# Kernel optimization log

Measured on AMD Instinct MI355X. Metric: run time of the kernel, lower is better.

Reference implementation:

```python
import jax, jax.numpy as jnp
import numpy as np

N_NODES = 50000


def gcn_conv(x, src, dst, W, b):
    # PyG GCNConv: x @ W, symmetric gcn_norm with self-loops, scatter-add, + bias
    n = x.shape[0]
    x = x @ W  # [N, out]
    deg = jax.ops.segment_sum(jnp.ones_like(src, dtype=x.dtype), dst, num_segments=n)
    dinv = jnp.where(deg > 0, deg ** -0.5, 0.0)
    norm = dinv[src] * dinv[dst]  # [E+N]
    out = jax.ops.segment_sum(x[src] * norm[:, None], dst, num_segments=n)
    return out + b


def setup_inputs() -> dict:
    key = jax.random.key(0)
    ks = jax.random.split(key, 8)
    x = jax.random.normal(ks[0], (N_NODES, 128), dtype=jnp.float32)
    edge_index = jax.random.randint(ks[1], (2, 800000), 0, N_NODES, dtype=jnp.int64)
    def glorot(k, fan_in, fan_out):
        s = (6.0 / (fan_in + fan_out)) ** 0.5
        return jax.random.uniform(k, (fan_in, fan_out), jnp.float32, -s, s)
    return {
        "x": x,
        "edge_index": edge_index,
        "W1": glorot(ks[2], 128, 128), "b1": jnp.zeros((128,), jnp.float32),
        "W2": glorot(ks[3], 128, 128), "b2": jnp.zeros((128,), jnp.float32),
        "W3": glorot(ks[4], 128, 64), "b3": jnp.zeros((64,), jnp.float32),
    }


def reference(x, edge_index, W1, b1, W2, b2, W3, b3):
    n = x.shape[0]
    loops = jnp.arange(n, dtype=edge_index.dtype)
    src = jnp.concatenate([edge_index[0], loops])  # self-loops appended
    dst = jnp.concatenate([edge_index[1], loops])
    h = gcn_conv(x, src, dst, W1, b1)
    h = jax.nn.relu(h)  # dropout is identity in eval mode
    h = gcn_conv(h, src, dst, W2, b2)
    h = jax.nn.relu(h)
    h = gcn_conv(h, src, dst, W3, b3)
    return h
```

## Files before the change

### kernel.cpp

```cpp
#include <hip/hip_runtime.h>
#include <hip/hip_bf16.h>
#include <hip/hip_fp16.h>


typedef __attribute__((ext_vector_type(8))) short s16x8;
typedef __attribute__((ext_vector_type(8))) unsigned short u16x8;
typedef __attribute__((ext_vector_type(4))) float f32x4;

__device__ __forceinline__ float bfu_lo(uint v) { return __uint_as_float(v << 16); }
__device__ __forceinline__ float bfu_hi(uint v) { return __uint_as_float(v & 0xffff0000u); }
__device__ __forceinline__ float dec_norm(uint m) {
    return __half2float(__ushort_as_half((ushort)(m >> 16)));
}
__device__ __forceinline__ ushort bf16_bits(float f) {
    union { __hip_bfloat16 h; ushort u; } x;
    x.h = __float2bfloat16(f);
    return x.u;
}


__global__ void k_init(int* __restrict__ deg, int n,
                       uint4* __restrict__ ep4, int cap4) {
    int i = blockIdx.x * blockDim.x + threadIdx.x;
    if (i < n) deg[i] = 1;
    if (i < cap4) ep4[i] = make_uint4(0u, 0u, 0u, 0u);
}

__global__ void k_hist(const int* __restrict__ dst, int E,
                       int* __restrict__ deg, ushort* __restrict__ rank) {
    int e = blockIdx.x * blockDim.x + threadIdx.x;
    if (e < E) {
        int r = atomicAdd(&deg[dst[e]], 1);
        rank[e] = (ushort)r;
    }
}

__global__ void k_scan_block(const int* __restrict__ deg, int* __restrict__ offs,
                             int* __restrict__ bsum, float* __restrict__ dinv, int n) {
    __shared__ int sm[256];
    int tid = threadIdx.x;
    int i = blockIdx.x * 256 + tid;
    int v = (i < n) ? deg[i] : 0;
    int pv = (i < n) ? ((v + 7) & ~7) : 0;
    if (i < n) dinv[i] = rsqrtf((float)v);
    sm[tid] = pv;
    __syncthreads();
    for (int off = 1; off < 256; off <<= 1) {
        int t = (tid >= off) ? sm[tid - off] : 0;
        __syncthreads();
        sm[tid] += t;
        __syncthreads();
    }
    if (i < n) offs[i] = sm[tid] - pv;
    if (tid == 255) bsum[blockIdx.x] = sm[255];
}

__global__ void k_scan_bsum(int* __restrict__ bsum, int nb, int* __restrict__ offs, int n) {
    __shared__ int sm[256];
    int tid = threadIdx.x;
    int v = (tid < nb) ? bsum[tid] : 0;
    sm[tid] = v;
    __syncthreads();
    for (int off = 1; off < 256; off <<= 1) {
        int t = (tid >= off) ? sm[tid - off] : 0;
        __syncthreads();
        sm[tid] += t;
        __syncthreads();
    }
    if (tid < nb) bsum[tid] = sm[tid] - v;
    if (tid == 255) offs[n] = sm[255];
}

__global__ void k_add_bsum(int* __restrict__ offs, const int* __restrict__ bsum, int n) {
    int i = blockIdx.x * blockDim.x + threadIdx.x;
    if (i < n) offs[i] += bsum[i >> 8];
}

__global__ __launch_bounds__(256) void k_fill(const int* __restrict__ src,
                                              const int* __restrict__ dst,
                                              const ushort* __restrict__ rank,
                                              int E, int n,
                                              const int* __restrict__ offs,
                                              const float* __restrict__ dinv,
                                              uint* __restrict__ ep) {
    int e = blockIdx.x * blockDim.x + threadIdx.x;
    int tot = E + n;
    if (e >= tot) return;
    int s, d, r;
    if (e < E) {
        s = src[e];
        d = dst[e];
        r = rank[e];
    } else {
        s = d = e - E;
        r = 0;
    }
    int pos = offs[d] + r;
    uint hb = (uint)__half_as_ushort(__float2half(dinv[s] * dinv[d]));
    ep[pos] = (hb << 16) | (uint)s;
}

__global__ void k_transW(const float* __restrict__ W1, const float* __restrict__ W2,
                         const float* __restrict__ W3,
                         ushort* __restrict__ Wt1, ushort* __restrict__ Wt2,
                         ushort* __restrict__ Wt3) {
    int i = blockIdx.x * 256 + threadIdx.x;
    if (i < 128 * 128) {
        int r = i >> 7, c = i & 127;
        Wt1[c * 128 + r] = bf16_bits(W1[i]);
        Wt2[c * 128 + r] = bf16_bits(W2[i]);
    }
    if (i < 128 * 64) {
        int r = i >> 6, c = i & 63;
        Wt3[c * 128 + r] = bf16_bits(W3[i]);
    }
}

template <int OUT, bool ABF16>
__global__ __launch_bounds__(256) void k_gemm_mfma(const void* __restrict__ Ain,
                                                   const ushort* __restrict__ Wt,
                                                   ushort* __restrict__ To, int n) {
    constexpr int NT = OUT / 16;
    __shared__ ushort As[64][136];
    __shared__ ushort Ws[OUT][136];
    const int tid = threadIdx.x;
    const int wave = tid >> 6, lane = tid & 63;
    const int m0 = blockIdx.x * 64;

#pragma unroll
    for (int it = 0; it < OUT / 16; ++it) {
        int idx = it * 256 + tid;
        int r = idx >> 4;
        int c8 = (idx & 15) << 3;
        *(u16x8*)&Ws[r][c8] = *(const u16x8*)(Wt + r * 128 + c8);
    }
    if constexpr (ABF16) {
        const ushort* A = (const ushort*)Ain;
#pragma unroll
        for (int it = 0; it < 4; ++it) {
            int idx = it * 256 + tid;
            int r = idx >> 4;
            int c8 = (idx & 15) << 3;
            u16x8 v = {0, 0, 0, 0, 0, 0, 0, 0};
            if (m0 + r < n) v = *(const u16x8*)(A + (size_t)(m0 + r) * 128 + c8);
            *(u16x8*)&As[r][c8] = v;
        }
    } else {
        const float* A = (const float*)Ain;
#pragma unroll
        for (int it = 0; it < 8; ++it) {
            int idx = it * 256 + tid;
            int r = idx >> 5;
            int c4 = (idx & 31) << 2;
            float4 v = make_float4(0.f, 0.f, 0.f, 0.f);
            if (m0 + r < n) v = *(const float4*)(A + (size_t)(m0 + r) * 128 + c4);
            As[r][c4 + 0] = bf16_bits(v.x);
            As[r][c4 + 1] = bf16_bits(v.y);
            As[r][c4 + 2] = bf16_bits(v.z);
            As[r][c4 + 3] = bf16_bits(v.w);
        }
    }
    __syncthreads();

    const int lrow = lane & 15;
    const int kgrp = lane >> 4;

    s16x8 a[4];
#pragma unroll
    for (int kk = 0; kk < 4; ++kk)
        a[kk] = *(const s16x8*)&As[wave * 16 + lrow][kk * 32 + kgrp * 8];

    f32x4 acc[NT];
#pragma unroll
    for (int nt = 0; nt < NT; ++nt) {
        f32x4 c = {0.f, 0.f, 0.f, 0.f};
#pragma unroll
        for (int kk = 0; kk < 4; ++kk) {
            s16x8 b = *(const s16x8*)&Ws[nt * 16 + lrow][kk * 32 + kgrp * 8];
            c = __builtin_amdgcn_mfma_f32_16x16x32_bf16(a[kk], b, c, 0, 0, 0);
        }
        acc[nt] = c;
    }

#pragma unroll
    for (int j = 0; j < 4; ++j) {
        int row = m0 + wave * 16 + kgrp * 4 + j;
        if (row < n) {
#pragma unroll
            for (int nt = 0; nt < NT; ++nt)
                To[(size_t)row * OUT + nt * 16 + lrow] = bf16_bits(acc[nt][j]);
        }
    }
}

template <bool RELU>
__global__ __launch_bounds__(256) void k_agg128(const ushort* __restrict__ T,
                                                const int* __restrict__ offs,
                                                const uint* __restrict__ ep,
                                                const float* __restrict__ bias,
                                                uint* __restrict__ outq, int n) {
    int pr = blockIdx.x * 4 + (threadIdx.x >> 6);
    int lane = threadIdx.x & 63;
    int w0 = pr * 2;
    if (w0 >= n) return;
    int w1 = w0 + 1;
    bool has1 = (w1 < n);
    int eA = offs[w0], endA = offs[w0 + 1];
    int eB = has1 ? offs[w1] : 0;
    int endB = has1 ? offs[w1 + 1] : 0;

    const uint* Tl = (const uint*)T + lane;
    const uint4 z4 = make_uint4(0u, 0u, 0u, 0u);
    float a0 = 0.f, a1 = 0.f, c0 = 0.f, c1 = 0.f;

    uint4 mA0 = *(const uint4*)(ep + eA);
    uint4 mA1 = *(const uint4*)(ep + eA + 4);
    uint4 mB0 = z4, mB1 = z4;
    if (eB < endB) { mB0 = *(const uint4*)(ep + eB); mB1 = *(const uint4*)(ep + eB + 4); }

    for (;;) {
        uint rA0 = Tl[(size_t)(mA0.x & 0xffffu) * 64];
        uint rA1 = Tl[(size_t)(mA0.y & 0xffffu) * 64];
        uint rA2 = Tl[(size_t)(mA0.z & 0xffffu) * 64];
        uint rA3 = Tl[(size_t)(mA0.w & 0xffffu) * 64];
        uint rA4 = Tl[(size_t)(mA1.x & 0xffffu) * 64];
        uint rA5 = Tl[(size_t)(mA1.y & 0xffffu) * 64];
        uint rA6 = Tl[(size_t)(mA1.z & 0xffffu) * 64];
        uint rA7 = Tl[(size_t)(mA1.w & 0xffffu) * 64];
        uint rB0 = Tl[(size_t)(mB0.x & 0xffffu) * 64];
        uint rB1 = Tl[(size_t)(mB0.y & 0xffffu) * 64];
        uint rB2 = Tl[(size_t)(mB0.z & 0xffffu) * 64];
        uint rB3 = Tl[(size_t)(mB0.w & 0xffffu) * 64];
        uint rB4 = Tl[(size_t)(mB1.x & 0xffffu) * 64];
        uint rB5 = Tl[(size_t)(mB1.y & 0xffffu) * 64];
        uint rB6 = Tl[(size_t)(mB1.z & 0xffffu) * 64];
        uint rB7 = Tl[(size_t)(mB1.w & 0xffffu) * 64];
        float wA0 = dec_norm(mA0.x), wA1 = dec_norm(mA0.y);
        float wA2 = dec_norm(mA0.z), wA3 = dec_norm(mA0.w);
        float wA4 = dec_norm(mA1.x), wA5 = dec_norm(mA1.y);
        float wA6 = dec_norm(mA1.z), wA7 = dec_norm(mA1.w);
        float wB0 = dec_norm(mB0.x), wB1 = dec_norm(mB0.y);
        float wB2 = dec_norm(mB0.z), wB3 = dec_norm(mB0.w);
        float wB4 = dec_norm(mB1.x), wB5 = dec_norm(mB1.y);
        float wB6 = dec_norm(mB1.z), wB7 = dec_norm(mB1.w);
        eA += 8;
        eB += 8;
        bool moreA = (eA < endA), moreB = (eB < endB);
        if (moreA) { mA0 = *(const uint4*)(ep + eA); mA1 = *(const uint4*)(ep + eA + 4); }
        else       { mA0 = z4; mA1 = z4; }
        if (moreB) { mB0 = *(const uint4*)(ep + eB); mB1 = *(const uint4*)(ep + eB + 4); }
        else       { mB0 = z4; mB1 = z4; }
        a0 += wA0 * bfu_lo(rA0); a1 += wA0 * bfu_hi(rA0);
        a0 += wA1 * bfu_lo(rA1); a1 += wA1 * bfu_hi(rA1);
        a0 += wA2 * bfu_lo(rA2); a1 += wA2 * bfu_hi(rA2);
        a0 += wA3 * bfu_lo(rA3); a1 += wA3 * bfu_hi(rA3);
        a0 += wA4 * bfu_lo(rA4); a1 += wA4 * bfu_hi(rA4);
        a0 += wA5 * bfu_lo(rA5); a1 += wA5 * bfu_hi(rA5);
        a0 += wA6 * bfu_lo(rA6); a1 += wA6 * bfu_hi(rA6);
        a0 += wA7 * bfu_lo(rA7); a1 += wA7 * bfu_hi(rA7);
        c0 += wB0 * bfu_lo(rB0); c1 += wB0 * bfu_hi(rB0);
        c0 += wB1 * bfu_lo(rB1); c1 += wB1 * bfu_hi(rB1);
        c0 += wB2 * bfu_lo(rB2); c1 += wB2 * bfu_hi(rB2);
        c0 += wB3 * bfu_lo(rB3); c1 += wB3 * bfu_hi(rB3);
        c0 += wB4 * bfu_lo(rB4); c1 += wB4 * bfu_hi(rB4);
        c0 += wB5 * bfu_lo(rB5); c1 += wB5 * bfu_hi(rB5);
        c0 += wB6 * bfu_lo(rB6); c1 += wB6 * bfu_hi(rB6);
        c0 += wB7 * bfu_lo(rB7); c1 += wB7 * bfu_hi(rB7);
        if (!moreA && !moreB) break;
    }

    float2 b = *(const float2*)(bias + (lane << 1));
    a0 += b.x; a1 += b.y;
    if (RELU) { a0 = fmaxf(a0, 0.f); a1 = fmaxf(a1, 0.f); }
    outq[(size_t)w0 * 64 + lane] = ((uint)bf16_bits(a1) << 16) | (uint)bf16_bits(a0);
    if (has1) {
        c0 += b.x; c1 += b.y;
        if (RELU) { c0 = fmaxf(c0, 0.f); c1 = fmaxf(c1, 0.f); }
        outq[(size_t)w1 * 64 + lane] = ((uint)bf16_bits(c1) << 16) | (uint)bf16_bits(c0);
    }
}

__global__ __launch_bounds__(256) void k_agg64(const ushort* __restrict__ T,
                                               const int* __restrict__ offs,
                                               const uint* __restrict__ ep,
                                               const float* __restrict__ bias,
                                               float* __restrict__ out, int n) {
    int pr = blockIdx.x * 4 + (threadIdx.x >> 6);
    int lane = threadIdx.x & 63;
    int w0 = pr * 2;
    if (w0 >= n) return;
    int w1 = w0 + 1;
    bool has1 = (w1 < n);
    int eA = offs[w0], endA = offs[w0 + 1];
    int eB = has1 ? offs[w1] : 0;
    int endB = has1 ? offs[w1 + 1] : 0;

    const ushort* Tl = T + lane;
    const uint4 z4 = make_uint4(0u, 0u, 0u, 0u);
    float a0 = 0.f, c0 = 0.f;

    uint4 mA0 = *(const uint4*)(ep + eA);
    uint4 mA1 = *(const uint4*)(ep + eA + 4);
    uint4 mB0 = z4, mB1 = z4;
    if (eB < endB) { mB0 = *(const uint4*)(ep + eB); mB1 = *(const uint4*)(ep + eB + 4); }

    for (;;) {
        float rA0 = __uint_as_float((uint)Tl[(size_t)(mA0.x & 0xffffu) * 64] << 16);
        float rA1 = __uint_as_float((uint)Tl[(size_t)(mA0.y & 0xffffu) * 64] << 16);
        float rA2 = __uint_as_float((uint)Tl[(size_t)(mA0.z & 0xffffu) * 64] << 16);
        float rA3 = __uint_as_float((uint)Tl[(size_t)(mA0.w & 0xffffu) * 64] << 16);
        float rA4 = __uint_as_float((uint)Tl[(size_t)(mA1.x & 0xffffu) * 64] << 16);
        float rA5 = __uint_as_float((uint)Tl[(size_t)(mA1.y & 0xffffu) * 64] << 16);
        float rA6 = __uint_as_float((uint)Tl[(size_t)(mA1.z & 0xffffu) * 64] << 16);
        float rA7 = __uint_as_float((uint)Tl[(size_t)(mA1.w & 0xffffu) * 64] << 16);
        float rB0 = __uint_as_float((uint)Tl[(size_t)(mB0.x & 0xffffu) * 64] << 16);
        float rB1 = __uint_as_float((uint)Tl[(size_t)(mB0.y & 0xffffu) * 64] << 16);
        float rB2 = __uint_as_float((uint)Tl[(size_t)(mB0.z & 0xffffu) * 64] << 16);
        float rB3 = __uint_as_float((uint)Tl[(size_t)(mB0.w & 0xffffu) * 64] << 16);
        float rB4 = __uint_as_float((uint)Tl[(size_t)(mB1.x & 0xffffu) * 64] << 16);
        float rB5 = __uint_as_float((uint)Tl[(size_t)(mB1.y & 0xffffu) * 64] << 16);
        float rB6 = __uint_as_float((uint)Tl[(size_t)(mB1.z & 0xffffu) * 64] << 16);
        float rB7 = __uint_as_float((uint)Tl[(size_t)(mB1.w & 0xffffu) * 64] << 16);
        float wA0 = dec_norm(mA0.x), wA1 = dec_norm(mA0.y);
        float wA2 = dec_norm(mA0.z), wA3 = dec_norm(mA0.w);
        float wA4 = dec_norm(mA1.x), wA5 = dec_norm(mA1.y);
        float wA6 = dec_norm(mA1.z), wA7 = dec_norm(mA1.w);
        float wB0 = dec_norm(mB0.x), wB1 = dec_norm(mB0.y);
        float wB2 = dec_norm(mB0.z), wB3 = dec_norm(mB0.w);
        float wB4 = dec_norm(mB1.x), wB5 = dec_norm(mB1.y);
        float wB6 = dec_norm(mB1.z), wB7 = dec_norm(mB1.w);
        eA += 8;
        eB += 8;
        bool moreA = (eA < endA), moreB = (eB < endB);
        if (moreA) { mA0 = *(const uint4*)(ep + eA); mA1 = *(const uint4*)(ep + eA + 4); }
        else       { mA0 = z4; mA1 = z4; }
        if (moreB) { mB0 = *(const uint4*)(ep + eB); mB1 = *(const uint4*)(ep + eB + 4); }
        else       { mB0 = z4; mB1 = z4; }
        a0 += wA0 * rA0 + wA1 * rA1 + wA2 * rA2 + wA3 * rA3;
        a0 += wA4 * rA4 + wA5 * rA5 + wA6 * rA6 + wA7 * rA7;
        c0 += wB0 * rB0 + wB1 * rB1 + wB2 * rB2 + wB3 * rB3;
        c0 += wB4 * rB4 + wB5 * rB5 + wB6 * rB6 + wB7 * rB7;
        if (!moreA && !moreB) break;
    }

    float bv = bias[lane];
    out[(size_t)w0 * 64 + lane] = a0 + bv;
    if (has1) out[(size_t)w1 * 64 + lane] = c0 + bv;
}


extern "C" void kernel_launch(void* const* d_in, const int* in_sizes, int n_in,
                              void* d_out, int out_size, void* d_ws, size_t ws_size,
                              hipStream_t stream) {
    const int n = in_sizes[0] / 128;
    const int E = in_sizes[1] / 2;

    const float* x  = (const float*)d_in[0];
    const int*   ei = (const int*)d_in[1];
    const float* W1 = (const float*)d_in[2];
    const float* b1 = (const float*)d_in[3];
    const float* W2 = (const float*)d_in[4];
    const float* b2 = (const float*)d_in[5];
    const float* W3 = (const float*)d_in[6];
    const float* b3 = (const float*)d_in[7];
    const int* src = ei;
    const int* dst = ei + E;
    float* out = (float*)d_out;

    const int cap = E + 8 * n;

    char* w = (char*)d_ws;
    auto alloc = [&](size_t bytes) {
        char* p = w;
        w += (bytes + 255) & ~(size_t)255;
        return p;
    };
    int*    deg    = (int*)alloc((size_t)n * 4);
    int*    offs   = (int*)alloc((size_t)(n + 1) * 4);
    int*    bsum   = (int*)alloc(256 * 4);
    float*  dinv   = (float*)alloc((size_t)n * 4);
    ushort* rank   = (ushort*)alloc((size_t)E * 2);
    uint*   ep     = (uint*)alloc((size_t)cap * 4);
    ushort* tA     = (ushort*)alloc((size_t)n * 128 * 2);
    uint*   hB     = (uint*)alloc((size_t)n * 64 * 4);
    ushort* Wt1    = (ushort*)alloc(128 * 128 * 2);
    ushort* Wt2    = (ushort*)alloc(128 * 128 * 2);
    ushort* Wt3    = (ushort*)alloc(64 * 128 * 2);

    const int nb = (n + 255) / 256;

    const int cap4 = (cap + 3) / 4;
    k_init<<<(cap4 + 255) / 256, 256, 0, stream>>>(deg, n, (uint4*)ep, cap4);
    k_transW<<<64, 256, 0, stream>>>(W1, W2, W3, Wt1, Wt2, Wt3);
    k_hist<<<(E + 255) / 256, 256, 0, stream>>>(dst, E, deg, rank);
    k_scan_block<<<nb, 256, 0, stream>>>(deg, offs, bsum, dinv, n);
    k_scan_bsum<<<1, 256, 0, stream>>>(bsum, nb, offs, n);
    k_add_bsum<<<nb, 256, 0, stream>>>(offs, bsum, n);
    k_fill<<<(E + n + 255) / 256, 256, 0, stream>>>(src, dst, rank, E, n, offs, dinv, ep);

    const int pair_blocks = ((n + 1) / 2 + 3) / 4;
    const int gemm_blocks = (n + 63) / 64;

    k_gemm_mfma<128, false><<<gemm_blocks, 256, 0, stream>>>(x, Wt1, tA, n);
    k_agg128<true><<<pair_blocks, 256, 0, stream>>>(tA, offs, ep, b1, hB, n);

    k_gemm_mfma<128, true><<<gemm_blocks, 256, 0, stream>>>(hB, Wt2, tA, n);
    k_agg128<true><<<pair_blocks, 256, 0, stream>>>(tA, offs, ep, b2, hB, n);

    k_gemm_mfma<64, true><<<gemm_blocks, 256, 0, stream>>>(hB, Wt3, tA, n);
    k_agg64<<<pair_blocks, 256, 0, stream>>>(tA, offs, ep, b3, out, n);
}
```

Measured before the change: 187.6 us.

## Fuse weight transpose into init, self-loops into scan, vectorize hist/fill and agg64

Merges the weight-transpose kernel into the init kernel. Self-loop CSR entries are now written in the offset-add pass, so the fill kernel handles only real edges, two per thread. The histogram also processes two edges per thread with vector loads. The final 64-wide aggregation now has each half-wave handle two destination nodes, loading two bf16 features per 32-bit gather. This cuts launch count and halves gather instructions in the last layer, at the cost of more register pressure and a less regular thread layout.

```diff
diff --git a/kernel.cpp b/kernel.cpp
--- a/kernel.cpp
+++ b/kernel.cpp
@@ -18,20 +18,37 @@
     return x.u;
 }
 
-
-__global__ void k_init(int* __restrict__ deg, int n,
+__global__ void k_init(const float* __restrict__ W1, const float* __restrict__ W2,
+                       const float* __restrict__ W3,
+                       ushort* __restrict__ Wt1, ushort* __restrict__ Wt2,
+                       ushort* __restrict__ Wt3,
+                       int* __restrict__ deg, int n,
                        uint4* __restrict__ ep4, int cap4) {
     int i = blockIdx.x * blockDim.x + threadIdx.x;
     if (i < n) deg[i] = 1;
     if (i < cap4) ep4[i] = make_uint4(0u, 0u, 0u, 0u);
+    if (i < 128 * 128) {
+        int r = i >> 7, c = i & 127;
+        Wt1[c * 128 + r] = bf16_bits(W1[i]);
+        Wt2[c * 128 + r] = bf16_bits(W2[i]);
+    }
+    if (i < 128 * 64) {
+        int r = i >> 6, c = i & 63;
+        Wt3[c * 128 + r] = bf16_bits(W3[i]);
+    }
 }
 
 __global__ void k_hist(const int* __restrict__ dst, int E,
                        int* __restrict__ deg, ushort* __restrict__ rank) {
-    int e = blockIdx.x * blockDim.x + threadIdx.x;
-    if (e < E) {
-        int r = atomicAdd(&deg[dst[e]], 1);
-        rank[e] = (ushort)r;
+    int e2 = (blockIdx.x * blockDim.x + threadIdx.x) * 2;
+    if (e2 >= E) return;
+    int2 d2 = *(const int2*)(dst + e2);
+    int r0 = atomicAdd(&deg[d2.x], 1);
+    if (e2 + 1 < E) {
+        int r1 = atomicAdd(&deg[d2.y], 1);
+        *(ushort2*)(rank + e2) = make_ushort2((ushort)r0, (ushort)r1);
+    } else {
+        rank[e2] = (ushort)r0;
     }
 }
 
@@ -71,48 +88,39 @@
     if (tid == 255) offs[n] = sm[255];
 }
 
-__global__ void k_add_bsum(int* __restrict__ offs, const int* __restrict__ bsum, int n) {
+__global__ void k_add_bsum(int* __restrict__ offs, const int* __restrict__ bsum,
+                           const float* __restrict__ dinv, uint* __restrict__ ep, int n) {
     int i = blockIdx.x * blockDim.x + threadIdx.x;
-    if (i < n) offs[i] += bsum[i >> 8];
+    if (i < n) {
+        int o = offs[i] + bsum[i >> 8];
+        offs[i] = o;
+        float dv = dinv[i];
+        uint hb = (uint)__half_as_ushort(__float2half(dv * dv));
+        ep[o] = (hb << 16) | (uint)i;
+    }
 }
 
 __global__ __launch_bounds__(256) void k_fill(const int* __restrict__ src,
                                               const int* __restrict__ dst,
                                               const ushort* __restrict__ rank,
-                                              int E, int n,
+                                              int E,
                                               const int* __restrict__ offs,
                                               const float* __restrict__ dinv,
                                               uint* __restrict__ ep) {
-    int e = blockIdx.x * blockDim.x + threadIdx.x;
-    int tot = E + n;
-    if (e >= tot) return;
-    int s, d, r;
-    if (e < E) {
-        s = src[e];
-        d = dst[e];
-        r = rank[e];
-    } else {
-        s = d = e - E;
-        r = 0;
-    }
-    int pos = offs[d] + r;
-    uint hb = (uint)__half_as_ushort(__float2half(dinv[s] * dinv[d]));
-    ep[pos] = (hb << 16) | (uint)s;
-}
-
-__global__ void k_transW(const float* __restrict__ W1, const float* __restrict__ W2,
-                         const float* __restrict__ W3,
-                         ushort* __restrict__ Wt1, ushort* __restrict__ Wt2,
-                         ushort* __restrict__ Wt3) {
-    int i = blockIdx.x * 256 + threadIdx.x;
-    if (i < 128 * 128) {
-        int r = i >> 7, c = i & 127;
-        Wt1[c * 128 + r] = bf16_bits(W1[i]);
-        Wt2[c * 128 + r] = bf16_bits(W2[i]);
-    }
-    if (i < 128 * 64) {
-        int r = i >> 6, c = i & 63;
-        Wt3[c * 128 + r] = bf16_bits(W3[i]);
+    int e2 = (blockIdx.x * blockDim.x + threadIdx.x) * 2;
+    if (e2 >= E) return;
+    int2 s2 = *(const int2*)(src + e2);
+    int2 d2 = *(const int2*)(dst + e2);
+    ushort2 r2 = *(const ushort2*)(rank + e2);
+    {
+        int pos = offs[d2.x] + (int)r2.x;
+        uint hb = (uint)__half_as_ushort(__float2half(dinv[s2.x] * dinv[d2.x]));
+        ep[pos] = (hb << 16) | (uint)s2.x;
+    }
+    if (e2 + 1 < E) {
+        int pos = offs[d2.y] + (int)r2.y;
+        uint hb = (uint)__half_as_ushort(__float2half(dinv[s2.y] * dinv[d2.y]));
+        ep[pos] = (hb << 16) | (uint)s2.y;
     }
 }
 
@@ -285,42 +293,43 @@
                                                const uint* __restrict__ ep,
                                                const float* __restrict__ bias,
                                                float* __restrict__ out, int n) {
-    int pr = blockIdx.x * 4 + (threadIdx.x >> 6);
+    int wv = blockIdx.x * 4 + (threadIdx.x >> 6);
     int lane = threadIdx.x & 63;
-    int w0 = pr * 2;
-    if (w0 >= n) return;
-    int w1 = w0 + 1;
-    bool has1 = (w1 < n);
-    int eA = offs[w0], endA = offs[w0 + 1];
-    int eB = has1 ? offs[w1] : 0;
-    int endB = has1 ? offs[w1 + 1] : 0;
-
-    const ushort* Tl = T + lane;
+    int half = lane >> 5;
+    int lh = lane & 31;
+    int base = wv * 4;
+    if (base >= n) return;
+    int wA = base + half * 2;
+    int wB = wA + 1;
+    int eA = 0, endA = 0, eB = 0, endB = 0;
+    if (wA < n) { eA = offs[wA]; endA = offs[wA + 1]; }
+    if (wB < n) { eB = offs[wB]; endB = offs[wB + 1]; }
+
+    const uint* Tl = (const uint*)T + lh;
     const uint4 z4 = make_uint4(0u, 0u, 0u, 0u);
-    float a0 = 0.f, c0 = 0.f;
-
-    uint4 mA0 = *(const uint4*)(ep + eA);
-    uint4 mA1 = *(const uint4*)(ep + eA + 4);
-    uint4 mB0 = z4, mB1 = z4;
+    float a0 = 0.f, a1 = 0.f, c0 = 0.f, c1 = 0.f;
+
+    uint4 mA0 = z4, mA1 = z4, mB0 = z4, mB1 = z4;
+    if (eA < endA) { mA0 = *(const uint4*)(ep + eA); mA1 = *(const uint4*)(ep + eA + 4); }
     if (eB < endB) { mB0 = *(const uint4*)(ep + eB); mB1 = *(const uint4*)(ep + eB + 4); }
 
     for (;;) {
-        float rA0 = __uint_as_float((uint)Tl[(size_t)(mA0.x & 0xffffu) * 64] << 16);
-        float rA1 = __uint_as_float((uint)Tl[(size_t)(mA0.y & 0xffffu) * 64] << 16);
-        float rA2 = __uint_as_float((uint)Tl[(size_t)(mA0.z & 0xffffu) * 64] << 16);
-        float rA3 = __uint_as_float((uint)Tl[(size_t)(mA0.w & 0xffffu) * 64] << 16);
-        float rA4 = __uint_as_float((uint)Tl[(size_t)(mA1.x & 0xffffu) * 64] << 16);
-        float rA5 = __uint_as_float((uint)Tl[(size_t)(mA1.y & 0xffffu) * 64] << 16);
-        float rA6 = __uint_as_float((uint)Tl[(size_t)(mA1.z & 0xffffu) * 64] << 16);
-        float rA7 = __uint_as_float((uint)Tl[(size_t)(mA1.w & 0xffffu) * 64] << 16);
-        float rB0 = __uint_as_float((uint)Tl[(size_t)(mB0.x & 0xffffu) * 64] << 16);
-        float rB1 = __uint_as_float((uint)Tl[(size_t)(mB0.y & 0xffffu) * 64] << 16);
-        float rB2 = __uint_as_float((uint)Tl[(size_t)(mB0.z & 0xffffu) * 64] << 16);
-        float rB3 = __uint_as_float((uint)Tl[(size_t)(mB0.w & 0xffffu) * 64] << 16);
-        float rB4 = __uint_as_float((uint)Tl[(size_t)(mB1.x & 0xffffu) * 64] << 16);
-        float rB5 = __uint_as_float((uint)Tl[(size_t)(mB1.y & 0xffffu) * 64] << 16);
-        float rB6 = __uint_as_float((uint)Tl[(size_t)(mB1.z & 0xffffu) * 64] << 16);
-        float rB7 = __uint_as_float((uint)Tl[(size_t)(mB1.w & 0xffffu) * 64] << 16);
+        uint rA0 = Tl[(size_t)(mA0.x & 0xffffu) * 32];
+        uint rA1 = Tl[(size_t)(mA0.y & 0xffffu) * 32];
+        uint rA2 = Tl[(size_t)(mA0.z & 0xffffu) * 32];
+        uint rA3 = Tl[(size_t)(mA0.w & 0xffffu) * 32];
+        uint rA4 = Tl[(size_t)(mA1.x & 0xffffu) * 32];
+        uint rA5 = Tl[(size_t)(mA1.y & 0xffffu) * 32];
+        uint rA6 = Tl[(size_t)(mA1.z & 0xffffu) * 32];
+        uint rA7 = Tl[(size_t)(mA1.w & 0xffffu) * 32];
+        uint rB0 = Tl[(size_t)(mB0.x & 0xffffu) * 32];
+        uint rB1 = Tl[(size_t)(mB0.y & 0xffffu) * 32];
+        uint rB2 = Tl[(size_t)(mB0.z & 0xffffu) * 32];
+        uint rB3 = Tl[(size_t)(mB0.w & 0xffffu) * 32];
+        uint rB4 = Tl[(size_t)(mB1.x & 0xffffu) * 32];
+        uint rB5 = Tl[(size_t)(mB1.y & 0xffffu) * 32];
+        uint rB6 = Tl[(size_t)(mB1.z & 0xffffu) * 32];
+        uint rB7 = Tl[(size_t)(mB1.w & 0xffffu) * 32];
         float wA0 = dec_norm(mA0.x), wA1 = dec_norm(mA0.y);
         float wA2 = dec_norm(mA0.z), wA3 = dec_norm(mA0.w);
         float wA4 = dec_norm(mA1.x), wA5 = dec_norm(mA1.y);
@@ -336,16 +345,30 @@
         else       { mA0 = z4; mA1 = z4; }
         if (moreB) { mB0 = *(const uint4*)(ep + eB); mB1 = *(const uint4*)(ep + eB + 4); }
         else       { mB0 = z4; mB1 = z4; }
-        a0 += wA0 * rA0 + wA1 * rA1 + wA2 * rA2 + wA3 * rA3;
-        a0 += wA4 * rA4 + wA5 * rA5 + wA6 * rA6 + wA7 * rA7;
-        c0 += wB0 * rB0 + wB1 * rB1 + wB2 * rB2 + wB3 * rB3;
-        c0 += wB4 * rB4 + wB5 * rB5 + wB6 * rB6 + wB7 * rB7;
+        a0 += wA0 * bfu_lo(rA0); a1 += wA0 * bfu_hi(rA0);
+        a0 += wA1 * bfu_lo(rA1); a1 += wA1 * bfu_hi(rA1);
+        a0 += wA2 * bfu_lo(rA2); a1 += wA2 * bfu_hi(rA2);
+        a0 += wA3 * bfu_lo(rA3); a1 += wA3 * bfu_hi(rA3);
+        a0 += wA4 * bfu_lo(rA4); a1 += wA4 * bfu_hi(rA4);
+        a0 += wA5 * bfu_lo(rA5); a1 += wA5 * bfu_hi(rA5);
+        a0 += wA6 * bfu_lo(rA6); a1 += wA6 * bfu_hi(rA6);
+        a0 += wA7 * bfu_lo(rA7); a1 += wA7 * bfu_hi(rA7);
+        c0 += wB0 * bfu_lo(rB0); c1 += wB0 * bfu_hi(rB0);
+        c0 += wB1 * bfu_lo(rB1); c1 += wB1 * bfu_hi(rB1);
+        c0 += wB2 * bfu_lo(rB2); c1 += wB2 * bfu_hi(rB2);
+        c0 += wB3 * bfu_lo(rB3); c1 += wB3 * bfu_hi(rB3);
+        c0 += wB4 * bfu_lo(rB4); c1 += wB4 * bfu_hi(rB4);
+        c0 += wB5 * bfu_lo(rB5); c1 += wB5 * bfu_hi(rB5);
+        c0 += wB6 * bfu_lo(rB6); c1 += wB6 * bfu_hi(rB6);
+        c0 += wB7 * bfu_lo(rB7); c1 += wB7 * bfu_hi(rB7);
         if (!moreA && !moreB) break;
     }
 
-    float bv = bias[lane];
-    out[(size_t)w0 * 64 + lane] = a0 + bv;
-    if (has1) out[(size_t)w1 * 64 + lane] = c0 + bv;
+    float2 b = *(const float2*)(bias + (lh << 1));
+    if (wA < n)
+        *(float2*)(out + (size_t)wA * 64 + (lh << 1)) = make_float2(a0 + b.x, a1 + b.y);
+    if (wB < n)
+        *(float2*)(out + (size_t)wB * 64 + (lh << 1)) = make_float2(c0 + b.x, c1 + b.y);
 }
 
 
@@ -390,15 +413,17 @@
     const int nb = (n + 255) / 256;
 
     const int cap4 = (cap + 3) / 4;
-    k_init<<<(cap4 + 255) / 256, 256, 0, stream>>>(deg, n, (uint4*)ep, cap4);
-    k_transW<<<64, 256, 0, stream>>>(W1, W2, W3, Wt1, Wt2, Wt3);
-    k_hist<<<(E + 255) / 256, 256, 0, stream>>>(dst, E, deg, rank);
+    const int init_n = max(cap4, n);
+    k_init<<<(init_n + 255) / 256, 256, 0, stream>>>(W1, W2, W3, Wt1, Wt2, Wt3,
+                                                     deg, n, (uint4*)ep, cap4);
+    k_hist<<<(E / 2 + 255) / 256, 256, 0, stream>>>(dst, E, deg, rank);
     k_scan_block<<<nb, 256, 0, stream>>>(deg, offs, bsum, dinv, n);
     k_scan_bsum<<<1, 256, 0, stream>>>(bsum, nb, offs, n);
-    k_add_bsum<<<nb, 256, 0, stream>>>(offs, bsum, n);
-    k_fill<<<(E + n + 255) / 256, 256, 0, stream>>>(src, dst, rank, E, n, offs, dinv, ep);
+    k_add_bsum<<<nb, 256, 0, stream>>>(offs, bsum, dinv, ep, n);
+    k_fill<<<(E / 2 + 255) / 256, 256, 0, stream>>>(src, dst, rank, E, offs, dinv, ep);
 
     const int pair_blocks = ((n + 1) / 2 + 3) / 4;
+    const int quad_blocks = ((n + 3) / 4 + 3) / 4;
     const int gemm_blocks = (n + 63) / 64;
 
     k_gemm_mfma<128, false><<<gemm_blocks, 256, 0, stream>>>(x, Wt1, tA, n);
@@ -408,5 +433,5 @@
     k_agg128<true><<<pair_blocks, 256, 0, stream>>>(tA, offs, ep, b2, hB, n);
 
     k_gemm_mfma<64, true><<<gemm_blocks, 256, 0, stream>>>(hB, Wt3, tA, n);
-    k_agg64<<<pair_blocks, 256, 0, stream>>>(tA, offs, ep, b3, out, n);
-}
+    k_agg64<<<quad_blocks, 256, 0, stream>>>(tA, offs, ep, b3, out, n);
+}
```

After: 181.6 us. 1.03x faster.
